# Kernel tuning notes

Measured on AMD Instinct MI355X. Metric: run time of the kernel, lower is better.

The kernel has to match this reference:

```python
import jax, jax.numpy as jnp
import numpy as np

K = 7        # kernal_size
STRIDE = 1
PAD = 3      # padding (reflect)
M = K // 2   # center tap index
GAMA = 0.5
EPS = 1e-09


def interp_linear(x, n_out):
    # torch F.interpolate(mode='linear', align_corners=False) on last dim. x: (b, c, n_in)
    n_in = x.shape[-1]
    src = (jnp.arange(n_out, dtype=jnp.float32) + 0.5) * (n_in / n_out) - 0.5
    src = jnp.clip(src, 0.0, n_in - 1.0)
    lo = jnp.floor(src).astype(jnp.int32)
    hi = jnp.minimum(lo + 1, n_in - 1)
    w = (src - lo.astype(jnp.float32)).astype(x.dtype)
    return x[..., lo] * (1.0 - w) + x[..., hi] * w


def unfold1d(x, k, s, p):
    # x: (b, c, n) -> windows (b, L, c, k), matching F.unfold's c-major/k-minor layout
    if p > 0:
        x = jnp.pad(x, ((0, 0), (0, 0), (p, p)), mode='reflect')
    n = x.shape[-1]
    L = (n - k) // s + 1
    idx = jnp.arange(L)[:, None] * s + jnp.arange(k)[None, :]  # (L, k)
    win = x[:, :, idx]                                          # (b, c, L, k)
    return jnp.transpose(win, (0, 2, 1, 3))                     # (b, L, c, k)


def setup_inputs() -> dict:
    key = jax.random.key(0)
    k1, k2, k3, k4, k5 = jax.random.split(key, 5)
    b, dc, nd = 16, 16, 1024
    c_in, c_out, n = 64, 128, 4096
    deep = jax.random.normal(k1, (b, dc, nd), dtype=jnp.float32)
    x = jax.random.normal(k2, (b, c_in, n), dtype=jnp.float32)
    conv_w = jax.random.normal(k3, (c_in, dc), dtype=jnp.float32) * (1.0 / np.sqrt(dc))
    conv_b = jax.random.normal(k4, (c_in,), dtype=jnp.float32) * 0.02
    fc_w = jax.random.normal(k5, (c_out, c_in * K), dtype=jnp.float32) * (1.0 / np.sqrt(c_in * K))
    return {"deep": deep, "x": x, "conv_w": conv_w, "conv_b": conv_b, "fc_w": fc_w}


def reference(deep, x, conv_w, conv_b, fc_w):
    b, c, n = x.shape
    # --- get_deep_loss ---
    xr = interp_linear(deep, n)                                  # (b, dc, n)
    y = jnp.einsum('bdn,cd->bcn', xr, conv_w) + conv_b[None, :, None]
    mean = jnp.mean(y, axis=2, keepdims=True)
    var = jnp.var(y, axis=2, keepdims=True, ddof=1)              # torch var_mean unbiased
    xs = GAMA * (y - mean) / (var + EPS)                         # DeepShuffle1d
    x1 = unfold1d(xs, K, STRIDE, PAD)                            # (b, L, c, k)
    d = jnp.abs(x1 - x1[..., M:M + 1])
    loss = 1.0 - jnp.tanh(d) ** 2                                # (b, L, c, k)
    alpha = 1.0 / jnp.sum(loss, axis=-1, keepdims=True)          # (b, L, c, 1)
    deep_loss = (loss * alpha).reshape(b, -1, c * K)             # (b, L, c*k)
    # --- deep_conv ---
    y1 = unfold1d(x, K, STRIDE, PAD).reshape(b, -1, c * K)       # (b, L, c*k)
    out = jnp.einsum('blf,of->bol', deep_loss * y1, fc_w)        # (b, c_out, L)
    return out
```

## Files before the change

kernel.cpp:

```cpp
#include <hip/hip_runtime.h>
#include <hip/hip_bf16.h>
#include <math.h>

namespace {
typedef __attribute__((ext_vector_type(8)))  short  short8;
typedef __attribute__((ext_vector_type(4)))  float  floatx4;

constexpr int Bc = 16;
constexpr int DC = 16;
constexpr int ND = 1024;
constexpr int C  = 64;
constexpr int N  = 4096;
constexpr int CO = 128;
constexpr int KW = 7;
constexpr int F  = C * KW;
constexpr int LT = 32;
constexpr int PLD = F + 8;
constexpr int GPS = 560;

constexpr size_t WB_OFF = 0;
constexpr size_t GP_OFF = 131072;
constexpr size_t XT_OFF = 524288;

__device__ inline unsigned short f2bf(float f) {
    __hip_bfloat16 h = __float2bfloat16(f);
    return __builtin_bit_cast(unsigned short, h);
}
__device__ inline float bf2f(unsigned short u) {
    unsigned int x = ((unsigned int)u) << 16;
    return __builtin_bit_cast(float, x);
}
__device__ inline float rcpf(float x) { return __builtin_amdgcn_rcpf(x); }
__device__ inline int reflect(int p) {
    p = (p < 0) ? -p : p;
    return (p >= N) ? (2 * N - 2 - p) : p;
}

__global__ __launch_bounds__(256)
void k0(const float* __restrict__ deep, const float* __restrict__ x,
        const float* __restrict__ fcw, unsigned short* __restrict__ wb,
        float* __restrict__ gp, unsigned short* __restrict__ xt)
{
    __shared__ __align__(16) char sm[9216];
    const int blk = blockIdx.x;
    const int tid = threadIdx.x;

    if (blk < 56) {
        const int i = (blk * 256 + tid) * 4;
        const float4 v = *(const float4*)(fcw + i);
        ushort4 o;
        o.x = f2bf(v.x); o.y = f2bf(v.y); o.z = f2bf(v.z); o.w = f2bf(v.w);
        *(ushort4*)(wb + i) = o;
        return;
    }
    if (blk < 184) {
        float (*Dch)[132] = (float (*)[132])sm;
        const int i2 = blk - 56;
        const int b  = i2 >> 3;
        const int ch = i2 & 7;
        const int t0 = ch * 128;
        const int d  = tid >> 4;
        const int e  = tid & 15;
#pragma unroll
        for (int p = 0; p < 9; ++p) {
            const int tt = e + 16 * p;
            if (tt < 129)
                Dch[d][tt] = deep[(b * DC + d) * ND + min(t0 + tt, ND - 1)];
        }
        __syncthreads();
        float a0 = 0.f, a1 = 0.f, as = 0.f;
        const int n1 = (ch == 7) ? 127 : 128;
        for (int t = 0; t < 128; ++t) {
            const float vd  = Dch[d][t];
            const float ve  = Dch[e][t];
            const float ve1 = (t < n1) ? Dch[e][t + 1] : 0.f;
            a0 = fmaf(vd, ve, a0);
            a1 = fmaf(vd, ve1, a1);
            as += vd;
        }
        float* gpb = gp + (b * 8 + ch) * GPS;
        gpb[tid] = a0;
        gpb[256 + tid] = a1;
        if (e == 0) {
            gpb[512 + d] = as;
            if (ch == 0) gpb[528 + d] = Dch[d][0];
            if (ch == 7) gpb[544 + d] = Dch[d][127];
        }
        return;
    }
    unsigned short (*xb)[72] = (unsigned short (*)[72])sm;
    const int i2 = blk - 184;
    const int b  = i2 >> 6;
    const int n0 = (i2 & 63) * 64;
    const int c  = tid >> 2;
    const int q  = tid & 3;
#pragma unroll
    for (int rep = 0; rep < 4; ++rep) {
        const int nl = q * 16 + rep * 4;
        const float4 v = *(const float4*)(x + (size_t)(b * C + c) * N + n0 + nl);
        xb[nl + 0][c] = f2bf(v.x);
        xb[nl + 1][c] = f2bf(v.y);
        xb[nl + 2][c] = f2bf(v.z);
        xb[nl + 3][c] = f2bf(v.w);
    }
    __syncthreads();
#pragma unroll
    for (int pass = 0; pass < 2; ++pass) {
        const int row  = (tid >> 3) + pass * 32;
        const int part = tid & 7;
        const uint4 v = *(const uint4*)(&xb[row][part * 8]);
        *(uint4*)(xt + (size_t)(b * N + n0 + row) * C + part * 8) = v;
    }
}

__global__ __launch_bounds__(256)
void k2(const float* __restrict__ deep, const float* __restrict__ conv_w,
        const float* __restrict__ conv_b, const float* __restrict__ gp,
        const unsigned short* __restrict__ xt, const unsigned short* __restrict__ wb,
        float* __restrict__ out)
{
    __shared__ __align__(16) char sm[40448];
    unsigned short* phi   = (unsigned short*)sm;
    float*          Dw    = (float*)sm;
    float*          qpart = (float*)(sm + 1024);
    unsigned short* xtile = (unsigned short*)(sm + 29184);
    float*          Vt    = (float*)(sm + 34048);
    float*          Gs    = (float*)(sm + 37120);
    float*          mcs   = (float*)(sm + 39360);
    float*          scs   = (float*)(sm + 39616);

    const int b   = blockIdx.y;
    const int l0  = blockIdx.x * LT;
    const int t0  = l0 >> 2;
    const int tid = threadIdx.x;
    const int c   = tid & 63;
    const int seg = tid >> 6;

    for (int u = tid; u < GPS; u += 256) {
        float v = 0.f;
        if (u < 528) {
#pragma unroll
            for (int ch = 0; ch < 8; ++ch) v += gp[(b * 8 + ch) * GPS + u];
        } else if (u < 544) {
            v = gp[(b * 8 + 0) * GPS + u];
        } else {
            v = gp[(b * 8 + 7) * GPS + u];
        }
        Gs[u] = v;
    }
    for (int u = tid; u < 38 * 8; u += 256) {
        const int row = u >> 3, part = u & 7;
        const int n = reflect(l0 - 3 + row);
        const uint4 v = *(const uint4*)(xt + (size_t)(b * N + n) * C + part * 8);
        *(uint4*)(xtile + row * 64 + part * 8) = v;
    }
    if (tid < 192) {
        const int ti = tid >> 4, d = tid & 15;
        const int t = min(max(t0 - 2 + ti, 0), ND - 1);
        Dw[ti * 16 + d] = deep[(b * DC + d) * ND + t];
    }
    __syncthreads();

    float w[DC];
    {
        const float4* wr = (const float4*)(conv_w + c * DC);
#pragma unroll
        for (int p = 0; p < 4; ++p) {
            const float4 v = wr[p];
            w[4 * p] = v.x; w[4 * p + 1] = v.y; w[4 * p + 2] = v.z; w[4 * p + 3] = v.w;
        }
    }
#pragma unroll
    for (int p = 0; p < 3; ++p) {
        const int ti = seg + 4 * p;
        float a = 0.f;
#pragma unroll
        for (int d = 0; d < DC; ++d) a = fmaf(w[d], Dw[ti * 16 + d], a);
        Vt[ti * 64 + c] = a;
    }
    {
        float q0 = 0.f, q1 = 0.f;
#pragma unroll
        for (int dd = 0; dd < 4; ++dd) {
            const int d = 4 * seg + dd;
            float i0 = 0.f, i1 = 0.f;
#pragma unroll
            for (int e = 0; e < DC; ++e) {
                i0 = fmaf(w[e], Gs[d * 16 + e], i0);
                i1 = fmaf(w[e], Gs[256 + d * 16 + e], i1);
            }
            q0 = fmaf(w[d], i0, q0);
            q1 = fmaf(w[d], i1, q1);
        }
        qpart[seg * 64 + c] = q0;
        qpart[256 + seg * 64 + c] = q1;
    }
    __syncthreads();

    if (tid < 64) {
        const float Q0 = qpart[c] + qpart[64 + c] + qpart[128 + c] + qpart[192 + c];
        const float Q1 = qpart[256 + c] + qpart[320 + c] + qpart[384 + c] + qpart[448 + c];
        float wS = 0.f, V0 = 0.f, VN = 0.f;
#pragma unroll
        for (int d = 0; d < DC; ++d) {
            wS = fmaf(w[d], Gs[512 + d], wS);
            V0 = fmaf(w[d], Gs[528 + d], V0);
            VN = fmaf(w[d], Gs[544 + d], VN);
        }
        const float cb   = conv_b[c];
        const float mean = wS * (1.f / 1024.f) + cb;
        const float S2   = 2.625f * Q0 + 1.375f * Q1 + 0.6875f * (V0 * V0 + VN * VN)
                         + 8.f * cb * wS + 4096.f * cb * cb;
        const float var  = (S2 - 4096.f * mean * mean) * (1.f / 4095.f);
        mcs[c] = wS * (1.f / 1024.f);
        scs[c] = 0.5f / (var + 1e-9f);
    }
    __syncthreads();

    {
        const int base = l0 + seg * 8;
        const float mc = mcs[c], sc = scs[c];
        float xsv[14], xvf[14];
#pragma unroll
        for (int i = 0; i < 14; ++i) {
            const int j  = base - 3 + i;
            const int ja = (j < 0) ? -j : j;
            const int jr = min(ja, 2 * N - 2 - ja);
            const int t  = jr >> 2;
            const int r  = jr & 3;
            const float wa = (r & 1) ? ((r & 2) ? 0.625f : 0.125f)
                                     : ((r & 2) ? 0.875f : 0.375f);
            int tA = t - 1 + (r >> 1);
            int tB = tA + 1;
            if (tA < 0) { tA = 0; tB = 0; }
            if (tB > ND - 1) tB = ND - 1;
            const int ia = tA - t0 + 2;
            const int ib = tB - t0 + 2;
            const float vl = wa * Vt[ia * 64 + c] + (1.f - wa) * Vt[ib * 64 + c];
            xsv[i] = (vl - mc) * sc;
            xvf[i] = bf2f(xtile[(seg * 8 + i) * 64 + c]);
        }
        unsigned short* pcol = phi + c * KW;
#pragma unroll
        for (int li = 0; li < 8; ++li) {
            const float cen = xsv[li + 3];
            float u[KW];
            float s = 0.25f;
            u[3] = 0.25f;
#pragma unroll
            for (int k = 0; k < KW; ++k) {
                if (k == 3) continue;
                const float d = fabsf(xsv[li + k] - cen);
                const float e = __expf(-2.f * d);
                const float t = 1.f + e;
                const float uk = e * rcpf(t * t);
                u[k] = uk;
                s += uk;
            }
            const float al = rcpf(s);
            unsigned short* pr = pcol + (seg * 8 + li) * PLD;
#pragma unroll
            for (int k = 0; k < KW; ++k) pr[k] = f2bf(u[k] * al * xvf[li + k]);
        }
    }
    __syncthreads();

    const int lane = tid & 63;
    const int quad = lane >> 4;
    const int rr   = lane & 15;
    const int o0   = seg * 32;

    floatx4 acc00 = {0.f, 0.f, 0.f, 0.f}, acc01 = acc00, acc10 = acc00, acc11 = acc00;
    const unsigned short* wrow0 = wb + (o0 + rr) * F + quad * 8;
    const unsigned short* wrow1 = wrow0 + 16 * F;
    const unsigned short* prow0 = phi + rr * PLD + quad * 8;
    const unsigned short* prow1 = prow0 + 16 * PLD;

    for (int s = 0; s < F / 32; ++s) {
        const int f0 = 32 * s;
        const short8 a0 = *(const short8*)(wrow0 + f0);
        const short8 a1 = *(const short8*)(wrow1 + f0);
        const short8 b0 = *(const short8*)(prow0 + f0);
        const short8 b1 = *(const short8*)(prow1 + f0);
        acc00 = __builtin_amdgcn_mfma_f32_16x16x32_bf16(a0, b0, acc00, 0, 0, 0);
        acc01 = __builtin_amdgcn_mfma_f32_16x16x32_bf16(a0, b1, acc01, 0, 0, 0);
        acc10 = __builtin_amdgcn_mfma_f32_16x16x32_bf16(a1, b0, acc10, 0, 0, 0);
        acc11 = __builtin_amdgcn_mfma_f32_16x16x32_bf16(a1, b1, acc11, 0, 0, 0);
    }

    float* ob = out + (size_t)(b * CO) * N + l0;
#pragma unroll
    for (int i = 0; i < 4; ++i) {
        const int om = quad * 4 + i;
        ob[(o0 + om) * N      + rr     ] = acc00[i];
        ob[(o0 + om) * N      + 16 + rr] = acc01[i];
        ob[(o0 + 16 + om) * N + rr     ] = acc10[i];
        ob[(o0 + 16 + om) * N + 16 + rr] = acc11[i];
    }
}
}

extern "C" void kernel_launch(void* const* d_in, const int* in_sizes, int n_in,
                              void* d_out, int out_size, void* d_ws, size_t ws_size,
                              hipStream_t stream)
{
    const float* deep   = (const float*)d_in[0];
    const float* x      = (const float*)d_in[1];
    const float* conv_w = (const float*)d_in[2];
    const float* conv_b = (const float*)d_in[3];
    const float* fc_w   = (const float*)d_in[4];
    float* out = (float*)d_out;

    unsigned short* wbuf = (unsigned short*)((char*)d_ws + WB_OFF);
    float*          gp   = (float*)((char*)d_ws + GP_OFF);
    unsigned short* xt   = (unsigned short*)((char*)d_ws + XT_OFF);

    hipLaunchKernelGGL(k0, dim3(56 + 128 + 1024), dim3(256), 0, stream,
                       deep, x, fc_w, wbuf, gp, xt);
    hipLaunchKernelGGL(k2, dim3(N / LT, Bc), dim3(256), 0, stream,
                       deep, conv_w, conv_b, gp, xt, wbuf, out);
}
```

Before: 129.1 us.

## Drop x transpose pass, read x directly, hoist per-channel stats into separate kernel

Removes the pre-pass that converted x into a transposed bf16 buffer. Each thread in the main kernel now reads its 14-sample window of x straight from the fp32 input with float4 loads, using a reflect-aware slow path only for edge blocks. The per-channel mean and scale reduction is moved out of every main-kernel block into a small per-batch kernel, so each block no longer re-reduces the Gram partials. The exponential is folded into exp2 via a prescaled factor, and launch bounds are raised to allow more occupancy. The cost is an extra kernel launch and uncoalesced-looking strided per-channel reads of x in the main kernel.

```diff
diff --git a/kernel.cpp b/kernel.cpp
--- a/kernel.cpp
+++ b/kernel.cpp
@@ -20,28 +20,22 @@
 
 constexpr size_t WB_OFF = 0;
 constexpr size_t GP_OFF = 131072;
-constexpr size_t XT_OFF = 524288;
+constexpr size_t MC_OFF = 417792;
+constexpr size_t SC_OFF = 421888;
+
+constexpr float EXP2_SCALE = 2.8853900817779268f;
 
 __device__ inline unsigned short f2bf(float f) {
     __hip_bfloat16 h = __float2bfloat16(f);
     return __builtin_bit_cast(unsigned short, h);
 }
-__device__ inline float bf2f(unsigned short u) {
-    unsigned int x = ((unsigned int)u) << 16;
-    return __builtin_bit_cast(float, x);
-}
 __device__ inline float rcpf(float x) { return __builtin_amdgcn_rcpf(x); }
-__device__ inline int reflect(int p) {
-    p = (p < 0) ? -p : p;
-    return (p >= N) ? (2 * N - 2 - p) : p;
-}
 
 __global__ __launch_bounds__(256)
-void k0(const float* __restrict__ deep, const float* __restrict__ x,
-        const float* __restrict__ fcw, unsigned short* __restrict__ wb,
-        float* __restrict__ gp, unsigned short* __restrict__ xt)
+void k0(const float* __restrict__ deep, const float* __restrict__ fcw,
+        unsigned short* __restrict__ wb, float* __restrict__ gp)
 {
-    __shared__ __align__(16) char sm[9216];
+    __shared__ __align__(16) float Dch[DC][132];
     const int blk = blockIdx.x;
     const int tid = threadIdx.x;
 
@@ -53,82 +47,119 @@
         *(ushort4*)(wb + i) = o;
         return;
     }
-    if (blk < 184) {
-        float (*Dch)[132] = (float (*)[132])sm;
-        const int i2 = blk - 56;
-        const int b  = i2 >> 3;
-        const int ch = i2 & 7;
-        const int t0 = ch * 128;
-        const int d  = tid >> 4;
-        const int e  = tid & 15;
-#pragma unroll
-        for (int p = 0; p < 9; ++p) {
-            const int tt = e + 16 * p;
-            if (tt < 129)
-                Dch[d][tt] = deep[(b * DC + d) * ND + min(t0 + tt, ND - 1)];
-        }
-        __syncthreads();
-        float a0 = 0.f, a1 = 0.f, as = 0.f;
-        const int n1 = (ch == 7) ? 127 : 128;
-        for (int t = 0; t < 128; ++t) {
-            const float vd  = Dch[d][t];
-            const float ve  = Dch[e][t];
-            const float ve1 = (t < n1) ? Dch[e][t + 1] : 0.f;
-            a0 = fmaf(vd, ve, a0);
-            a1 = fmaf(vd, ve1, a1);
-            as += vd;
-        }
-        float* gpb = gp + (b * 8 + ch) * GPS;
-        gpb[tid] = a0;
-        gpb[256 + tid] = a1;
-        if (e == 0) {
-            gpb[512 + d] = as;
-            if (ch == 0) gpb[528 + d] = Dch[d][0];
-            if (ch == 7) gpb[544 + d] = Dch[d][127];
-        }
-        return;
-    }
-    unsigned short (*xb)[72] = (unsigned short (*)[72])sm;
-    const int i2 = blk - 184;
-    const int b  = i2 >> 6;
-    const int n0 = (i2 & 63) * 64;
-    const int c  = tid >> 2;
-    const int q  = tid & 3;
-#pragma unroll
-    for (int rep = 0; rep < 4; ++rep) {
-        const int nl = q * 16 + rep * 4;
-        const float4 v = *(const float4*)(x + (size_t)(b * C + c) * N + n0 + nl);
-        xb[nl + 0][c] = f2bf(v.x);
-        xb[nl + 1][c] = f2bf(v.y);
-        xb[nl + 2][c] = f2bf(v.z);
-        xb[nl + 3][c] = f2bf(v.w);
-    }
-    __syncthreads();
-#pragma unroll
-    for (int pass = 0; pass < 2; ++pass) {
-        const int row  = (tid >> 3) + pass * 32;
-        const int part = tid & 7;
-        const uint4 v = *(const uint4*)(&xb[row][part * 8]);
-        *(uint4*)(xt + (size_t)(b * N + n0 + row) * C + part * 8) = v;
+    const int i2 = blk - 56;
+    const int b  = i2 >> 3;
+    const int ch = i2 & 7;
+    const int t0 = ch * 128;
+    const int d  = tid >> 4;
+    const int e  = tid & 15;
+#pragma unroll
+    for (int p = 0; p < 9; ++p) {
+        const int tt = e + 16 * p;
+        if (tt < 129)
+            Dch[d][tt] = deep[(b * DC + d) * ND + min(t0 + tt, ND - 1)];
+    }
+    __syncthreads();
+    float a0 = 0.f, a1 = 0.f, as = 0.f;
+    const int n1 = (ch == 7) ? 127 : 128;
+    for (int t = 0; t < 128; ++t) {
+        const float vd  = Dch[d][t];
+        const float ve  = Dch[e][t];
+        const float ve1 = (t < n1) ? Dch[e][t + 1] : 0.f;
+        a0 = fmaf(vd, ve, a0);
+        a1 = fmaf(vd, ve1, a1);
+        as += vd;
+    }
+    float* gpb = gp + (b * 8 + ch) * GPS;
+    gpb[tid] = a0;
+    gpb[256 + tid] = a1;
+    if (e == 0) {
+        gpb[512 + d] = as;
+        if (ch == 0) gpb[528 + d] = Dch[d][0];
+        if (ch == 7) gpb[544 + d] = Dch[d][127];
     }
 }
 
 __global__ __launch_bounds__(256)
+void ks(const float* __restrict__ gp, const float* __restrict__ conv_w,
+        const float* __restrict__ conv_b, float* __restrict__ mcs,
+        float* __restrict__ scs)
+{
+    __shared__ float G0s[256], G1s[256], ss[16], dd0[16], ddN[16], qp[8][64];
+    const int b = blockIdx.x, tid = threadIdx.x;
+    {
+        float a0 = 0.f, a1 = 0.f;
+#pragma unroll
+        for (int ch = 0; ch < 8; ++ch) {
+            const float* gpb = gp + (b * 8 + ch) * GPS;
+            a0 += gpb[tid];
+            a1 += gpb[256 + tid];
+        }
+        G0s[tid] = a0; G1s[tid] = a1;
+        if (tid < 16) {
+            float s = 0.f;
+#pragma unroll
+            for (int ch = 0; ch < 8; ++ch) s += gp[(b * 8 + ch) * GPS + 512 + tid];
+            ss[tid]  = s;
+            dd0[tid] = gp[(b * 8 + 0) * GPS + 528 + tid];
+            ddN[tid] = gp[(b * 8 + 7) * GPS + 544 + tid];
+        }
+    }
+    __syncthreads();
+    const int c = tid & 63, part = tid >> 6;
+    float w[DC];
+    {
+        const float4* wr = (const float4*)(conv_w + c * DC);
+#pragma unroll
+        for (int p = 0; p < 4; ++p) {
+            const float4 v = wr[p];
+            w[4 * p] = v.x; w[4 * p + 1] = v.y; w[4 * p + 2] = v.z; w[4 * p + 3] = v.w;
+        }
+    }
+    float q0 = 0.f, q1 = 0.f;
+#pragma unroll
+    for (int dd = 0; dd < 4; ++dd) {
+        const int d = 4 * part + dd;
+        float i0 = 0.f, i1 = 0.f;
+#pragma unroll
+        for (int e = 0; e < DC; ++e) {
+            i0 = fmaf(w[e], G0s[d * 16 + e], i0);
+            i1 = fmaf(w[e], G1s[d * 16 + e], i1);
+        }
+        q0 = fmaf(w[d], i0, q0);
+        q1 = fmaf(w[d], i1, q1);
+    }
+    qp[part][c] = q0;
+    qp[4 + part][c] = q1;
+    __syncthreads();
+    if (tid < 64) {
+        const float Q0 = qp[0][c] + qp[1][c] + qp[2][c] + qp[3][c];
+        const float Q1 = qp[4][c] + qp[5][c] + qp[6][c] + qp[7][c];
+        float wS = 0.f, V0 = 0.f, VN = 0.f;
+#pragma unroll
+        for (int d = 0; d < DC; ++d) {
+            wS = fmaf(w[d], ss[d],  wS);
+            V0 = fmaf(w[d], dd0[d], V0);
+            VN = fmaf(w[d], ddN[d], VN);
+        }
+        const float cb   = conv_b[c];
+        const float mean = wS * (1.f / 1024.f) + cb;
+        const float S2   = 2.625f * Q0 + 1.375f * Q1 + 0.6875f * (V0 * V0 + VN * VN)
+                         + 8.f * cb * wS + 4096.f * cb * cb;
+        const float var  = (S2 - 4096.f * mean * mean) * (1.f / 4095.f);
+        mcs[b * 64 + c] = wS * (1.f / 1024.f);
+        scs[b * 64 + c] = (0.5f / (var + 1e-9f)) * EXP2_SCALE;
+    }
+}
+
+__global__ __launch_bounds__(256, 4)
 void k2(const float* __restrict__ deep, const float* __restrict__ conv_w,
-        const float* __restrict__ conv_b, const float* __restrict__ gp,
-        const unsigned short* __restrict__ xt, const unsigned short* __restrict__ wb,
+        const float* __restrict__ x, const float* __restrict__ mcs,
+        const float* __restrict__ scs, const unsigned short* __restrict__ wb,
         float* __restrict__ out)
 {
-    __shared__ __align__(16) char sm[40448];
-    unsigned short* phi   = (unsigned short*)sm;
-    float*          Dw    = (float*)sm;
-    float*          qpart = (float*)(sm + 1024);
-    unsigned short* xtile = (unsigned short*)(sm + 29184);
-    float*          Vt    = (float*)(sm + 34048);
-    float*          Gs    = (float*)(sm + 37120);
-    float*          mcs   = (float*)(sm + 39360);
-    float*          scs   = (float*)(sm + 39616);
-
+    __shared__ __align__(16) unsigned short phi[LT * PLD];
+    __shared__ __align__(16) float Dw[12 * 16];
     const int b   = blockIdx.y;
     const int l0  = blockIdx.x * LT;
     const int t0  = l0 >> 2;
@@ -136,31 +167,11 @@
     const int c   = tid & 63;
     const int seg = tid >> 6;
 
-    for (int u = tid; u < GPS; u += 256) {
-        float v = 0.f;
-        if (u < 528) {
-#pragma unroll
-            for (int ch = 0; ch < 8; ++ch) v += gp[(b * 8 + ch) * GPS + u];
-        } else if (u < 544) {
-            v = gp[(b * 8 + 0) * GPS + u];
-        } else {
-            v = gp[(b * 8 + 7) * GPS + u];
-        }
-        Gs[u] = v;
-    }
-    for (int u = tid; u < 38 * 8; u += 256) {
-        const int row = u >> 3, part = u & 7;
-        const int n = reflect(l0 - 3 + row);
-        const uint4 v = *(const uint4*)(xt + (size_t)(b * N + n) * C + part * 8);
-        *(uint4*)(xtile + row * 64 + part * 8) = v;
-    }
     if (tid < 192) {
         const int ti = tid >> 4, d = tid & 15;
         const int t = min(max(t0 - 2 + ti, 0), ND - 1);
         Dw[ti * 16 + d] = deep[(b * DC + d) * ND + t];
     }
-    __syncthreads();
-
     float w[DC];
     {
         const float4* wr = (const float4*)(conv_w + c * DC);
@@ -170,75 +181,60 @@
             w[4 * p] = v.x; w[4 * p + 1] = v.y; w[4 * p + 2] = v.z; w[4 * p + 3] = v.w;
         }
     }
-#pragma unroll
-    for (int p = 0; p < 3; ++p) {
-        const int ti = seg + 4 * p;
-        float a = 0.f;
-#pragma unroll
-        for (int d = 0; d < DC; ++d) a = fmaf(w[d], Dw[ti * 16 + d], a);
-        Vt[ti * 64 + c] = a;
-    }
-    {
-        float q0 = 0.f, q1 = 0.f;
-#pragma unroll
-        for (int dd = 0; dd < 4; ++dd) {
-            const int d = 4 * seg + dd;
-            float i0 = 0.f, i1 = 0.f;
-#pragma unroll
-            for (int e = 0; e < DC; ++e) {
-                i0 = fmaf(w[e], Gs[d * 16 + e], i0);
-                i1 = fmaf(w[e], Gs[256 + d * 16 + e], i1);
-            }
-            q0 = fmaf(w[d], i0, q0);
-            q1 = fmaf(w[d], i1, q1);
-        }
-        qpart[seg * 64 + c] = q0;
-        qpart[256 + seg * 64 + c] = q1;
-    }
-    __syncthreads();
-
-    if (tid < 64) {
-        const float Q0 = qpart[c] + qpart[64 + c] + qpart[128 + c] + qpart[192 + c];
-        const float Q1 = qpart[256 + c] + qpart[320 + c] + qpart[384 + c] + qpart[448 + c];
-        float wS = 0.f, V0 = 0.f, VN = 0.f;
-#pragma unroll
-        for (int d = 0; d < DC; ++d) {
-            wS = fmaf(w[d], Gs[512 + d], wS);
-            V0 = fmaf(w[d], Gs[528 + d], V0);
-            VN = fmaf(w[d], Gs[544 + d], VN);
-        }
-        const float cb   = conv_b[c];
-        const float mean = wS * (1.f / 1024.f) + cb;
-        const float S2   = 2.625f * Q0 + 1.375f * Q1 + 0.6875f * (V0 * V0 + VN * VN)
-                         + 8.f * cb * wS + 4096.f * cb * cb;
-        const float var  = (S2 - 4096.f * mean * mean) * (1.f / 4095.f);
-        mcs[c] = wS * (1.f / 1024.f);
-        scs[c] = 0.5f / (var + 1e-9f);
-    }
+    const float mc  = mcs[b * 64 + c];
+    const float sc2 = scs[b * 64 + c];
     __syncthreads();
 
     {
         const int base = l0 + seg * 8;
-        const float mc = mcs[c], sc = scs[c];
+        float Vr[6];
+#pragma unroll
+        for (int m = 0; m < 6; ++m) {
+            const float* dr = Dw + (2 * seg + m) * 16;
+            float a = 0.f;
+#pragma unroll
+            for (int d = 0; d < DC; ++d) a = fmaf(w[d], dr[d], a);
+            Vr[m] = a;
+        }
+        const float WA[4] = {0.375f, 0.125f, 0.875f, 0.625f};
         float xsv[14], xvf[14];
-#pragma unroll
-        for (int i = 0; i < 14; ++i) {
-            const int j  = base - 3 + i;
-            const int ja = (j < 0) ? -j : j;
-            const int jr = min(ja, 2 * N - 2 - ja);
-            const int t  = jr >> 2;
-            const int r  = jr & 3;
-            const float wa = (r & 1) ? ((r & 2) ? 0.625f : 0.125f)
-                                     : ((r & 2) ? 0.875f : 0.375f);
-            int tA = t - 1 + (r >> 1);
-            int tB = tA + 1;
-            if (tA < 0) { tA = 0; tB = 0; }
-            if (tB > ND - 1) tB = ND - 1;
-            const int ia = tA - t0 + 2;
-            const int ib = tB - t0 + 2;
-            const float vl = wa * Vt[ia * 64 + c] + (1.f - wa) * Vt[ib * 64 + c];
-            xsv[i] = (vl - mc) * sc;
-            xvf[i] = bf2f(xtile[(seg * 8 + i) * 64 + c]);
+        const bool edge = (blockIdx.x == 0 && seg == 0) ||
+                          (blockIdx.x == (N / LT - 1) && seg == 3);
+        const float* xr = x + (size_t)(b * C + c) * N;
+        if (!edge) {
+            const float4 x0 = *(const float4*)(xr + base - 4);
+            const float4 x1 = *(const float4*)(xr + base);
+            const float4 x2 = *(const float4*)(xr + base + 4);
+            const float4 x3 = *(const float4*)(xr + base + 8);
+            const float xf[16] = {x0.x, x0.y, x0.z, x0.w, x1.x, x1.y, x1.z, x1.w,
+                                  x2.x, x2.y, x2.z, x2.w, x3.x, x3.y, x3.z, x3.w};
+#pragma unroll
+            for (int i = 0; i < 14; ++i) {
+                const int r  = (i + 1) & 3;
+                const int ma = ((i + 5) >> 2) - 1 + (r >> 1);
+                const float wa = WA[r];
+                xsv[i] = (fmaf(wa, Vr[ma], (1.f - wa) * Vr[ma + 1]) - mc) * sc2;
+                xvf[i] = xf[1 + i];
+            }
+        } else {
+            const int tbase = t0 + 2 * seg - 2;
+#pragma unroll
+            for (int i = 0; i < 14; ++i) {
+                const int j  = base - 3 + i;
+                const int ja = (j < 0) ? -j : j;
+                const int jr = min(ja, 2 * N - 2 - ja);
+                const int t  = jr >> 2;
+                const int r  = jr & 3;
+                const float wa = WA[r];
+                int tA = t - 1 + (r >> 1);
+                int tB = tA + 1;
+                if (tA < 0) { tA = 0; tB = 0; }
+                if (tB > ND - 1) tB = ND - 1;
+                const int ia = tA - tbase;
+                const int ib = tB - tbase;
+                xsv[i] = (wa * Vr[ia] + (1.f - wa) * Vr[ib] - mc) * sc2;
+                xvf[i] = xr[jr];
+            }
         }
         unsigned short* pcol = phi + c * KW;
 #pragma unroll
@@ -251,7 +247,7 @@
             for (int k = 0; k < KW; ++k) {
                 if (k == 3) continue;
                 const float d = fabsf(xsv[li + k] - cen);
-                const float e = __expf(-2.f * d);
+                const float e = __builtin_amdgcn_exp2f(-d);
                 const float t = 1.f + e;
                 const float uk = e * rcpf(t * t);
                 u[k] = uk;
@@ -313,10 +309,13 @@
 
     unsigned short* wbuf = (unsigned short*)((char*)d_ws + WB_OFF);
     float*          gp   = (float*)((char*)d_ws + GP_OFF);
-    unsigned short* xt   = (unsigned short*)((char*)d_ws + XT_OFF);
-
-    hipLaunchKernelGGL(k0, dim3(56 + 128 + 1024), dim3(256), 0, stream,
-                       deep, x, fc_w, wbuf, gp, xt);
+    float*          mcs  = (float*)((char*)d_ws + MC_OFF);
+    float*          scs  = (float*)((char*)d_ws + SC_OFF);
+
+    hipLaunchKernelGGL(k0, dim3(56 + 128), dim3(256), 0, stream,
+                       deep, fc_w, wbuf, gp);
+    hipLaunchKernelGGL(ks, dim3(Bc), dim3(256), 0, stream,
+                       gp, conv_w, conv_b, mcs, scs);
     hipLaunchKernelGGL(k2, dim3(N / LT, Bc), dim3(256), 0, stream,
-                       deep, conv_w, conv_b, gp, xt, wbuf, out);
-}
+                       deep, conv_w, x, mcs, scs, wbuf, out);
+}
```

Result: slower. 134.5 us (+4.2%).
